# Performance work log

Hardware: AMD Instinct MI355X
Metric: run time of the kernel (lower is better)

## Reference

```python
import jax, jax.numpy as jnp
import numpy as np

V = 8192
E = 262144
IN_DIM = 128
OUT_DIM = 128
NEG_SLOPE = 0.2


def setup_inputs() -> dict:
    key = jax.random.key(0)
    k1, k2, k3, k4 = jax.random.split(key, 4)
    h = jax.random.normal(k1, (V, IN_DIM), dtype=jnp.float32)
    edge_index = jax.random.randint(k2, (2, E), 0, V, dtype=jnp.int64)
    # nn.Linear weights: W (out_dim, in_dim), att (1, 2*out_dim), both bias-free
    W = jax.random.normal(k3, (OUT_DIM, IN_DIM), dtype=jnp.float32) / np.sqrt(IN_DIM)
    att_w = jax.random.normal(k4, (1, 2 * OUT_DIM), dtype=jnp.float32) / np.sqrt(2 * OUT_DIM)
    return {"h": h, "edge_index": edge_index, "W": W, "att_w": att_w}


def reference(h, edge_index, W, att_w):
    # h: (V, in_dim) -> (V, out_dim)
    hw = h @ W.T
    src, dst = edge_index[0], edge_index[1]
    # edge features: concat of endpoint embeddings -> (E, 2*out_dim)
    e = jnp.concatenate([hw[src], hw[dst]], axis=-1)
    # attention logits per edge, LeakyReLU(0.2)
    a = jax.nn.leaky_relu(jnp.squeeze(e @ att_w.T, -1), negative_slope=NEG_SLOPE)
    v = hw.shape[0]
    # faithful to original: dense V x V matrix, zeros on non-edges,
    # softmax over ALL columns (non-edges included as score 0)
    alpha = jnp.zeros((v, v), dtype=hw.dtype).at[src, dst].set(a)
    alpha = jax.nn.softmax(alpha, axis=-1)
    # dropout is identity in eval mode (deterministic reference)
    return alpha @ hw
```

## Files before the change

kernel.cpp:

```cpp
#include <hip/hip_runtime.h>
#include <hip/hip_bf16.h>
#include <math.h>


#define V 8192
#define E 262144
#define D 128
#define NEG_SLOPE 0.2f
#define CAP 96
#define CSTRIDE 16

#define FMA4(acc, hv, wv) { acc.x += (hv)*(wv).x; acc.y += (hv)*(wv).y; \
                            acc.z += (hv)*(wv).z; acc.w += (hv)*(wv).w; }

__device__ __forceinline__ unsigned short f2bf(float f) {
    unsigned u = __float_as_uint(f);
    return (unsigned short)((u + 0x7fffu + ((u >> 16) & 1u)) >> 16);
}
__device__ __forceinline__ float bf2f_low(int p) {
    return __uint_as_float(((unsigned)p) << 16);
}

__global__ __launch_bounds__(256) void k_hw(const float* __restrict__ h,
                                            const float* __restrict__ W,
                                            const float* __restrict__ att,
                                            unsigned short* __restrict__ hwb,
                                            float* __restrict__ s1,
                                            float* __restrict__ s2,
                                            float* __restrict__ Pb,
                                            int* __restrict__ cnt) {
    __shared__ float Wt[D * 132];
    __shared__ float atts[2 * D];
    __shared__ float scr[8 * D];
    int t = threadIdx.x, b = blockIdx.x;
    int g = b * 256 + t;
    cnt[g] = 0;
    cnt[g + V * CSTRIDE / 2] = 0;
    atts[t] = att[t];
    for (int f4 = t; f4 < (D * D) / 4; f4 += 256) {
        int o = f4 >> 5, k = (f4 & 31) * 4;
        float4 wv = *(const float4*)&W[o * D + k];
        Wt[(k + 0) * 132 + o] = wv.x;
        Wt[(k + 1) * 132 + o] = wv.y;
        Wt[(k + 2) * 132 + o] = wv.z;
        Wt[(k + 3) * 132 + o] = wv.w;
    }
    __syncthreads();

    int c4 = (t & 31) * 4;
    int rq = t >> 5;
    int r0 = b * 32;
    float4 a0 = make_float4(0.f,0.f,0.f,0.f), a1 = a0, a2 = a0, a3 = a0;
    const float* h0p = &h[(r0 + rq     ) * D];
    const float* h1p = &h[(r0 + rq +  8) * D];
    const float* h2p = &h[(r0 + rq + 16) * D];
    const float* h3p = &h[(r0 + rq + 24) * D];
    #pragma unroll 4
    for (int kq = 0; kq < D; kq += 4) {
        float4 w0 = *(const float4*)&Wt[(kq + 0) * 132 + c4];
        float4 w1 = *(const float4*)&Wt[(kq + 1) * 132 + c4];
        float4 w2 = *(const float4*)&Wt[(kq + 2) * 132 + c4];
        float4 w3 = *(const float4*)&Wt[(kq + 3) * 132 + c4];
        float4 hv;
        hv = *(const float4*)&h0p[kq];
        FMA4(a0, hv.x, w0); FMA4(a0, hv.y, w1); FMA4(a0, hv.z, w2); FMA4(a0, hv.w, w3);
        hv = *(const float4*)&h1p[kq];
        FMA4(a1, hv.x, w0); FMA4(a1, hv.y, w1); FMA4(a1, hv.z, w2); FMA4(a1, hv.w, w3);
        hv = *(const float4*)&h2p[kq];
        FMA4(a2, hv.x, w0); FMA4(a2, hv.y, w1); FMA4(a2, hv.z, w2); FMA4(a2, hv.w, w3);
        hv = *(const float4*)&h3p[kq];
        FMA4(a3, hv.x, w0); FMA4(a3, hv.y, w1); FMA4(a3, hv.z, w2); FMA4(a3, hv.w, w3);
    }
    *(ushort4*)&hwb[(r0 + rq     ) * D + c4] = make_ushort4(f2bf(a0.x), f2bf(a0.y), f2bf(a0.z), f2bf(a0.w));
    *(ushort4*)&hwb[(r0 + rq +  8) * D + c4] = make_ushort4(f2bf(a1.x), f2bf(a1.y), f2bf(a1.z), f2bf(a1.w));
    *(ushort4*)&hwb[(r0 + rq + 16) * D + c4] = make_ushort4(f2bf(a2.x), f2bf(a2.y), f2bf(a2.z), f2bf(a2.w));
    *(ushort4*)&hwb[(r0 + rq + 24) * D + c4] = make_ushort4(f2bf(a3.x), f2bf(a3.y), f2bf(a3.z), f2bf(a3.w));

    float q1[4], q2[4];
    float4* accs[4] = {&a0, &a1, &a2, &a3};
    #pragma unroll
    for (int r = 0; r < 4; ++r) {
        float4 v = *accs[r];
        q1[r] = v.x * atts[c4] + v.y * atts[c4 + 1] + v.z * atts[c4 + 2] + v.w * atts[c4 + 3];
        q2[r] = v.x * atts[D + c4] + v.y * atts[D + c4 + 1] + v.z * atts[D + c4 + 2] + v.w * atts[D + c4 + 3];
    }
    #pragma unroll
    for (int m = 16; m; m >>= 1) {
        #pragma unroll
        for (int r = 0; r < 4; ++r) {
            q1[r] += __shfl_xor(q1[r], m);
            q2[r] += __shfl_xor(q2[r], m);
        }
    }
    if ((t & 31) == 0) {
        #pragma unroll
        for (int r = 0; r < 4; ++r) {
            s1[r0 + rq + r * 8] = q1[r];
            s2[r0 + rq + r * 8] = q2[r];
        }
    }

    scr[rq * D + c4 + 0] = a0.x + a1.x + a2.x + a3.x;
    scr[rq * D + c4 + 1] = a0.y + a1.y + a2.y + a3.y;
    scr[rq * D + c4 + 2] = a0.z + a1.z + a2.z + a3.z;
    scr[rq * D + c4 + 3] = a0.w + a1.w + a2.w + a3.w;
    __syncthreads();
    if (t < D) {
        float s = 0.f;
        #pragma unroll
        for (int r = 0; r < 8; ++r) s += scr[r * D + t];
        Pb[b * D + t] = s;
    }
}

__global__ __launch_bounds__(256) void k_scatter(const int* __restrict__ ei,
                                                 const float* __restrict__ s1,
                                                 const float* __restrict__ s2,
                                                 int* __restrict__ cnt,
                                                 int* __restrict__ bucket,
                                                 const float* __restrict__ Pb,
                                                 float* __restrict__ S) {
    int b = blockIdx.x, t = threadIdx.x;
    if (b < 1024) {
        int g = b * 256 + t;
        int src = ei[g];
        int dst = ei[E + g];
        float a = s1[src] + s2[dst];
        a = a > 0.f ? a : NEG_SLOPE * a;
        float w = expf(a) - 1.f;
        int pos = atomicAdd(&cnt[src * CSTRIDE], 1);
        if (pos < CAP)
            bucket[src * CAP + pos] = (dst << 16) | (int)f2bf(w);
    } else {
        __shared__ float red[256];
        int c = t & 127, half = t >> 7;
        float s = 0.f;
        #pragma unroll 4
        for (int r = half; r < 256; r += 2)
            s += Pb[r * D + c];
        red[t] = s;
        __syncthreads();
        if (t < D) S[t] = red[t] + red[D + t];
    }
}

__global__ __launch_bounds__(256) void k_row(const int* __restrict__ bucket,
                                             const int* __restrict__ cnt,
                                             const unsigned short* __restrict__ hwb,
                                             const float* __restrict__ S,
                                             float* __restrict__ out) {
    __shared__ int lb[4][CAP];
    int t = threadIdx.x;
    int wv = t >> 6, lane = t & 63;
    int row = blockIdx.x * 4 + wv;
    int deg = cnt[row * CSTRIDE];
    if (deg > CAP) deg = CAP;
    const int* bk = bucket + row * CAP;
    int e0 = bk[lane];
    int e1 = (lane < CAP - 64) ? bk[64 + lane] : 0;
    int p0 = (lane < deg)      ? e0 : (int)0xFFFF0000;
    int p1 = (64 + lane < deg) ? e1 : (int)0xFFFF0000;
    lb[wv][lane] = p0;
    if (lane < CAP - 64) lb[wv][64 + lane] = p1;
    int d0 = p0 >> 16;
    int d1 = p1 >> 16;
    int n0 = deg < 64 ? deg : 64;
    float accx = 0.f, accy = 0.f, dex = 0.f;
    const int* myb = lb[wv];
    int col2 = lane * 2;
    int j = 0;
    for (; j + 8 <= n0; j += 8) {
        int4 pa = *(const int4*)&myb[j];
        int4 pb = *(const int4*)&myb[j + 4];
        int da0 = pa.x >> 16, da1 = pa.y >> 16, da2 = pa.z >> 16, da3 = pa.w >> 16;
        int db0 = pb.x >> 16, db1 = pb.y >> 16, db2 = pb.z >> 16, db3 = pb.w >> 16;
        unsigned ha0 = *(const unsigned*)&hwb[da0 * D + col2];
        unsigned ha1 = *(const unsigned*)&hwb[da1 * D + col2];
        unsigned ha2 = *(const unsigned*)&hwb[da2 * D + col2];
        unsigned ha3 = *(const unsigned*)&hwb[da3 * D + col2];
        unsigned hb0 = *(const unsigned*)&hwb[db0 * D + col2];
        unsigned hb1 = *(const unsigned*)&hwb[db1 * D + col2];
        unsigned hb2 = *(const unsigned*)&hwb[db2 * D + col2];
        unsigned hb3 = *(const unsigned*)&hwb[db3 * D + col2];
        unsigned long long ma0 = __ballot(d0 == da0);
        unsigned long long ma1 = __ballot(d0 == da1);
        unsigned long long ma2 = __ballot(d0 == da2);
        unsigned long long ma3 = __ballot(d0 == da3);
        unsigned long long mb0 = __ballot(d0 == db0);
        unsigned long long mb1 = __ballot(d0 == db1);
        unsigned long long mb2 = __ballot(d0 == db2);
        unsigned long long mb3 = __ballot(d0 == db3);
        float wa0 = (ma0 & ((1ull << (j + 0)) - 1ull)) ? 0.f : bf2f_low(pa.x);
        float wa1 = (ma1 & ((1ull << (j + 1)) - 1ull)) ? 0.f : bf2f_low(pa.y);
        float wa2 = (ma2 & ((1ull << (j + 2)) - 1ull)) ? 0.f : bf2f_low(pa.z);
        float wa3 = (ma3 & ((1ull << (j + 3)) - 1ull)) ? 0.f : bf2f_low(pa.w);
        float wb0 = (mb0 & ((1ull << (j + 4)) - 1ull)) ? 0.f : bf2f_low(pb.x);
        float wb1 = (mb1 & ((1ull << (j + 5)) - 1ull)) ? 0.f : bf2f_low(pb.y);
        float wb2 = (mb2 & ((1ull << (j + 6)) - 1ull)) ? 0.f : bf2f_low(pb.z);
        float wb3 = (mb3 & ((1ull << (j + 7)) - 1ull)) ? 0.f : bf2f_low(pb.w);
        accx += wa0 * __uint_as_float(ha0 << 16);
        accy += wa0 * __uint_as_float(ha0 & 0xFFFF0000u);
        accx += wa1 * __uint_as_float(ha1 << 16);
        accy += wa1 * __uint_as_float(ha1 & 0xFFFF0000u);
        accx += wa2 * __uint_as_float(ha2 << 16);
        accy += wa2 * __uint_as_float(ha2 & 0xFFFF0000u);
        accx += wa3 * __uint_as_float(ha3 << 16);
        accy += wa3 * __uint_as_float(ha3 & 0xFFFF0000u);
        accx += wb0 * __uint_as_float(hb0 << 16);
        accy += wb0 * __uint_as_float(hb0 & 0xFFFF0000u);
        accx += wb1 * __uint_as_float(hb1 << 16);
        accy += wb1 * __uint_as_float(hb1 & 0xFFFF0000u);
        accx += wb2 * __uint_as_float(hb2 << 16);
        accy += wb2 * __uint_as_float(hb2 & 0xFFFF0000u);
        accx += wb3 * __uint_as_float(hb3 << 16);
        accy += wb3 * __uint_as_float(hb3 & 0xFFFF0000u);
        dex += wa0 + wa1 + wa2 + wa3 + wb0 + wb1 + wb2 + wb3;
    }
    for (; j < n0; ++j) {
        int pj = myb[j];
        int dj = pj >> 16;
        float wj = bf2f_low(pj);
        unsigned long long m = __ballot(d0 == dj);
        if (m & ((1ull << j) - 1ull)) wj = 0.f;
        unsigned hv = *(const unsigned*)&hwb[dj * D + col2];
        accx += wj * __uint_as_float(hv << 16);
        accy += wj * __uint_as_float(hv & 0xFFFF0000u);
        dex += wj;
    }
    for (j = 64; j < deg; ++j) {
        int pj = myb[j];
        int dj = pj >> 16;
        float wj = bf2f_low(pj);
        unsigned long long m0 = __ballot(d0 == dj);
        unsigned long long m1 = __ballot(d1 == dj) & ((1ull << (j - 64)) - 1ull);
        if (m0 | m1) wj = 0.f;
        unsigned hv = *(const unsigned*)&hwb[dj * D + col2];
        accx += wj * __uint_as_float(hv << 16);
        accy += wj * __uint_as_float(hv & 0xFFFF0000u);
        dex += wj;
    }
    float inv = 1.f / ((float)V + dex);
    float2 s = *(const float2*)&S[col2];
    float2 o;
    o.x = (s.x + accx) * inv;
    o.y = (s.y + accy) * inv;
    *(float2*)&out[row * D + col2] = o;
}

extern "C" void kernel_launch(void* const* d_in, const int* in_sizes, int n_in,
                              void* d_out, int out_size, void* d_ws, size_t ws_size,
                              hipStream_t stream) {
    const float* h   = (const float*)d_in[0];
    const int*   ei  = (const int*)d_in[1];
    const float* W   = (const float*)d_in[2];
    const float* att = (const float*)d_in[3];
    float* out = (float*)d_out;

    char* ws = (char*)d_ws;
    unsigned short* hwb = (unsigned short*)(ws);
    float* s1  = (float*)(ws + 2097152);
    float* s2  = (float*)(ws + 2129920);
    float* S   = (float*)(ws + 2162688);
    int*   cnt = (int*)(ws + 2163200);
    int*   bucket = (int*)(ws + 2687488);
    float* Pb  = (float*)(ws + 5833216);

    k_hw     <<<256,  256, 0, stream>>>(h, W, att, hwb, s1, s2, Pb, cnt);
    k_scatter<<<1025, 256, 0, stream>>>(ei, s1, s2, cnt, bucket, Pb, S);
    k_row    <<<2048, 256, 0, stream>>>(bucket, cnt, hwb, S, out);
}
```

Measured before the change: 105.7 us.

## Move edge-weight computation into row kernel and split each row across two waves

The scatter kernel now stores only the destination index per edge, so it no longer does random gathers of s1/s2 or computes exp. The row kernel computes the LeakyReLU/exp weights per bucket entry while loading the bucket. Each row is now handled by two wavefronts that interleave the edge chunks, and their partial sums are combined through shared memory. This adds a block-wide barrier and a second reduction step, and doubles the block count, in exchange for more parallelism per row and less latency per wave.

After: 109.4 us. +3.4%, slower.

```diff
diff --git a/kernel.cpp b/kernel.cpp
--- a/kernel.cpp
+++ b/kernel.cpp
@@ -114,8 +114,6 @@
 }
 
 __global__ __launch_bounds__(256) void k_scatter(const int* __restrict__ ei,
-                                                 const float* __restrict__ s1,
-                                                 const float* __restrict__ s2,
                                                  int* __restrict__ cnt,
                                                  int* __restrict__ bucket,
                                                  const float* __restrict__ Pb,
@@ -125,12 +123,9 @@
         int g = b * 256 + t;
         int src = ei[g];
         int dst = ei[E + g];
-        float a = s1[src] + s2[dst];
-        a = a > 0.f ? a : NEG_SLOPE * a;
-        float w = expf(a) - 1.f;
         int pos = atomicAdd(&cnt[src * CSTRIDE], 1);
         if (pos < CAP)
-            bucket[src * CAP + pos] = (dst << 16) | (int)f2bf(w);
+            bucket[src * CAP + pos] = dst;
     } else {
         __shared__ float red[256];
         int c = t & 127, half = t >> 7;
@@ -147,29 +142,47 @@
 __global__ __launch_bounds__(256) void k_row(const int* __restrict__ bucket,
                                              const int* __restrict__ cnt,
                                              const unsigned short* __restrict__ hwb,
+                                             const float* __restrict__ s1,
+                                             const float* __restrict__ s2,
                                              const float* __restrict__ S,
                                              float* __restrict__ out) {
-    __shared__ int lb[4][CAP];
+    __shared__ int   lb[2][CAP];
+    __shared__ float racc[2][2][D];
+    __shared__ float rdex[2][2];
     int t = threadIdx.x;
     int wv = t >> 6, lane = t & 63;
-    int row = blockIdx.x * 4 + wv;
+    int rsel = wv >> 1;
+    int wh = wv & 1;
+    int row = blockIdx.x * 2 + rsel;
     int deg = cnt[row * CSTRIDE];
     if (deg > CAP) deg = CAP;
     const int* bk = bucket + row * CAP;
     int e0 = bk[lane];
-    int e1 = (lane < CAP - 64) ? bk[64 + lane] : 0;
-    int p0 = (lane < deg)      ? e0 : (int)0xFFFF0000;
-    int p1 = (64 + lane < deg) ? e1 : (int)0xFFFF0000;
-    lb[wv][lane] = p0;
-    if (lane < CAP - 64) lb[wv][64 + lane] = p1;
-    int d0 = p0 >> 16;
-    int d1 = p1 >> 16;
+    int e1 = (lane < CAP - 64) ? bk[64 + lane] : -1;
+    int d0 = (lane < deg)      ? e0 : -1;
+    int d1 = (64 + lane < deg) ? e1 : -1;
+    float s1r = s1[row];
+    float s20 = (d0 >= 0) ? s2[d0] : 0.f;
+    float s21 = (d1 >= 0) ? s2[d1] : 0.f;
+    float aa0 = s1r + s20; aa0 = aa0 > 0.f ? aa0 : NEG_SLOPE * aa0;
+    float aa1 = s1r + s21; aa1 = aa1 > 0.f ? aa1 : NEG_SLOPE * aa1;
+    float w0 = expf(aa0) - 1.f;
+    float w1 = expf(aa1) - 1.f;
+    if (d0 < 0) w0 = 0.f;
+    if (d1 < 0) w1 = 0.f;
+    int p0 = (d0 << 16) | (int)f2bf(w0);
+    int p1 = (d1 << 16) | (int)f2bf(w1);
+    if (wh == 0) {
+        lb[rsel][lane] = p0;
+        if (lane < CAP - 64) lb[rsel][64 + lane] = p1;
+    }
+    __syncthreads();
+
     int n0 = deg < 64 ? deg : 64;
     float accx = 0.f, accy = 0.f, dex = 0.f;
-    const int* myb = lb[wv];
+    const int* myb = lb[rsel];
     int col2 = lane * 2;
-    int j = 0;
-    for (; j + 8 <= n0; j += 8) {
+    for (int j = wh * 8; j + 8 <= n0; j += 16) {
         int4 pa = *(const int4*)&myb[j];
         int4 pb = *(const int4*)&myb[j + 4];
         int da0 = pa.x >> 16, da1 = pa.y >> 16, da2 = pa.z >> 16, da3 = pa.w >> 16;
@@ -216,7 +229,8 @@
         accy += wb3 * __uint_as_float(hb3 & 0xFFFF0000u);
         dex += wa0 + wa1 + wa2 + wa3 + wb0 + wb1 + wb2 + wb3;
     }
-    for (; j < n0; ++j) {
+    int nb8 = n0 & ~7;
+    for (int j = nb8 + wh; j < n0; j += 2) {
         int pj = myb[j];
         int dj = pj >> 16;
         float wj = bf2f_low(pj);
@@ -227,7 +241,7 @@
         accy += wj * __uint_as_float(hv & 0xFFFF0000u);
         dex += wj;
     }
-    for (j = 64; j < deg; ++j) {
+    for (int j = 64 + wh; j < deg; j += 2) {
         int pj = myb[j];
         int dj = pj >> 16;
         float wj = bf2f_low(pj);
@@ -239,12 +253,22 @@
         accy += wj * __uint_as_float(hv & 0xFFFF0000u);
         dex += wj;
     }
-    float inv = 1.f / ((float)V + dex);
-    float2 s = *(const float2*)&S[col2];
-    float2 o;
-    o.x = (s.x + accx) * inv;
-    o.y = (s.y + accy) * inv;
-    *(float2*)&out[row * D + col2] = o;
+
+    racc[rsel][wh][col2]     = accx;
+    racc[rsel][wh][col2 + 1] = accy;
+    if (lane == 0) rdex[rsel][wh] = dex;
+    __syncthreads();
+    if (wh == 0) {
+        float ax = racc[rsel][0][col2]     + racc[rsel][1][col2];
+        float ay = racc[rsel][0][col2 + 1] + racc[rsel][1][col2 + 1];
+        float dexT = rdex[rsel][0] + rdex[rsel][1];
+        float inv = 1.f / ((float)V + dexT);
+        float2 s = *(const float2*)&S[col2];
+        float2 o;
+        o.x = (s.x + ax) * inv;
+        o.y = (s.y + ay) * inv;
+        *(float2*)&out[row * D + col2] = o;
+    }
 }
 
 extern "C" void kernel_launch(void* const* d_in, const int* in_sizes, int n_in,
@@ -266,6 +290,6 @@
     float* Pb  = (float*)(ws + 5833216);
 
     k_hw     <<<256,  256, 0, stream>>>(h, W, att, hwb, s1, s2, Pb, cnt);
-    k_scatter<<<1025, 256, 0, stream>>>(ei, s1, s2, cnt, bucket, Pb, S);
-    k_row    <<<2048, 256, 0, stream>>>(bucket, cnt, hwb, S, out);
-}
+    k_scatter<<<1025, 256, 0, stream>>>(ei, cnt, bucket, Pb, S);
+    k_row    <<<4096, 256, 0, stream>>>(bucket, cnt, hwb, s1, s2, S, out);
+}
```
